# Performance work log

Measured on AMD Instinct MI355X. Metric: run time of the kernel, lower is better.

Reference implementation:

```python
import jax, jax.numpy as jnp
import numpy as np

SUB_NO = 20
T_NO = 200
T_DATA = 200000
E_NO = 400
I_NO = 100
N_BASIS = 20
COS_SHIFT = 1.0
COS_SCALE = 5.0


def make_cos_basis():
    # (N_BASIS, T_NO) raised-cosine basis in log time
    i = jnp.arange(N_BASIS, dtype=jnp.float32)[:, None]
    phi = (jnp.pi / 2.0) * i
    x = jnp.arange(T_NO, dtype=jnp.float32)[None, :]
    raw = COS_SCALE * jnp.log(x + COS_SHIFT)
    basis = 0.5 * jnp.cos(raw - phi) + 0.5
    keep = (raw >= phi - jnp.pi) & (raw <= phi + jnp.pi)
    return jnp.where(keep, basis, 0.0)


def grouped_causal_conv(syn, kern_flipped):
    # syn: (T, sub), kern_flipped: (sub, T_NO) already time-reversed -> causal filter
    x = jnp.pad(syn.T, ((0, 0), (T_NO - 1, 0)))[None]          # (1, sub, T+T_NO-1)
    out = jax.lax.conv_general_dilated(
        x, kern_flipped[:, None, :], (1,), 'VALID',
        dimension_numbers=('NCH', 'OIH', 'NCH'),
        feature_group_count=syn.shape[1])
    return out[0].T                                             # (T, sub)


def causal_conv1(z_pad, kern_flipped):
    # z_pad: (L,), kern_flipped: (T_NO,) -> valid conv, length L - T_NO + 1
    out = jax.lax.conv_general_dilated(
        z_pad[None, None, :], kern_flipped[None, None, :], (1,), 'VALID',
        dimension_numbers=('NCH', 'OIH', 'NCH'))
    return out[0, 0]


def setup_inputs() -> dict:
    key = jax.random.key(0)
    ks = jax.random.split(key, 12)
    S_e = (jax.random.uniform(ks[0], (T_DATA, E_NO)) < 0.05).astype(jnp.float32)
    S_i = (jax.random.uniform(ks[1], (T_DATA, I_NO)) < 0.05).astype(jnp.float32)
    Z = (jax.random.uniform(ks[2], (T_DATA,)) < 0.02).astype(jnp.float32)
    # binary-tree dendrite adjacency
    C_den = np.zeros((SUB_NO, SUB_NO), dtype=np.int32)
    for c in range(1, SUB_NO):
        C_den[(c - 1) // 2, c] = 1
    C_den = jnp.asarray(C_den)
    e_asn = np.asarray(jax.random.randint(ks[3], (E_NO,), 0, SUB_NO))
    i_asn = np.asarray(jax.random.randint(ks[4], (I_NO,), 0, SUB_NO))
    C_syn_e = np.zeros((SUB_NO, E_NO), dtype=np.float32); C_syn_e[e_asn, np.arange(E_NO)] = 1.0
    C_syn_i = np.zeros((SUB_NO, I_NO), dtype=np.float32); C_syn_i[i_asn, np.arange(I_NO)] = 1.0
    W_syn_ns = jax.random.uniform(ks[5], (SUB_NO, 2)) * 0.1
    W_syn_ns = W_syn_ns.at[:, 1].multiply(-1.0)
    return {
        'S_e': S_e, 'S_i': S_i, 'Z': Z,
        'C_den': C_den,
        'C_syn_e': jnp.asarray(C_syn_e), 'C_syn_i': jnp.asarray(C_syn_i),
        'W_syn_ns': W_syn_ns,
        'Tau_syn_ns': jnp.ones((SUB_NO, 2)) * 3.0,
        'Delta_syn_ns': jnp.zeros((SUB_NO, 2)),
        'W_syn_s': jax.random.normal(ks[6], (SUB_NO, N_BASIS, 2)) * 0.01,
        'W_sub_ns': jnp.ones(SUB_NO) * 0.1,
        'W_sub_s': jnp.ones(SUB_NO) * 0.1,
        'V_o': jax.random.normal(ks[7], (1,)),
        'Theta_ns': jnp.zeros(SUB_NO),
        'Theta_s': jnp.zeros(SUB_NO),
        'hist_s_weights': jax.random.normal(ks[8], (N_BASIS,)) * 0.01,
        'hist_ns_weights': jax.random.normal(ks[9], (N_BASIS,)) * 0.01,
    }


def reference(S_e, S_i, Z, C_den, C_syn_e, C_syn_i, W_syn_ns, Tau_syn_ns,
              Delta_syn_ns, W_syn_s, W_sub_ns, W_sub_s, V_o, Theta_ns,
              Theta_s, hist_s_weights, hist_ns_weights):
    cos_basis = make_cos_basis()
    # --- spike_convolve ---
    syn_e = S_e @ C_syn_e.T                                     # (T, sub)
    syn_i = S_i @ C_syn_i.T
    t = jnp.arange(T_NO, dtype=jnp.float32)[None, :]
    tau_e = Tau_syn_ns[:, 0:1] ** 2
    tau_i = Tau_syn_ns[:, 1:2] ** 2
    t_e = jnp.maximum(t - Delta_syn_ns[:, 0:1], 0.0) / tau_e
    t_i = jnp.maximum(t - Delta_syn_ns[:, 1:2], 0.0) / tau_i
    e_kern_ns = t_e * jnp.exp(-t_e) * W_syn_ns[:, 0:1] ** 2      # (sub, T_NO)
    i_kern_ns = -t_i * jnp.exp(-t_i) * W_syn_ns[:, 1:2] ** 2
    e_kern_s = (W_syn_s[:, :, 0] ** 2) @ cos_basis               # (sub, T_NO)
    i_kern_s = -(W_syn_s[:, :, 1] ** 2) @ cos_basis
    filt_e_ns = grouped_causal_conv(syn_e, jnp.flip(e_kern_ns, 1))
    filt_i_ns = grouped_causal_conv(syn_i, jnp.flip(i_kern_ns, 1))
    filt_e_s = grouped_causal_conv(syn_e, jnp.flip(e_kern_s, 1))
    filt_i_s = grouped_causal_conv(syn_i, jnp.flip(i_kern_s, 1))
    syn_ns = filt_e_ns + filt_i_ns
    syn_s = filt_e_s + filt_i_s
    # --- spike-history filtering of observed root spikes Z ---
    hist_s_kern = hist_s_weights @ cos_basis                     # (T_NO,)
    hist_ns_kern = hist_ns_weights @ cos_basis
    Z_pad = jnp.pad(Z, (T_NO, 0))                                # (T + T_NO,)
    hist_ns_filt = causal_conv1(Z_pad, jnp.flip(hist_ns_kern))[:-1]  # (T,)
    hist_s_filt = causal_conv1(Z_pad, jnp.flip(hist_s_kern))[:-1]
    # --- leaf-to-root tree recursion (unrolled over SUB_NO static nodes) ---
    C_den_f = C_den.astype(syn_s.dtype)
    w_s2 = W_sub_s ** 2
    w_ns2 = W_sub_ns ** 2
    T_data = S_e.shape[0]
    s_out = jnp.zeros((T_data, SUB_NO), dtype=syn_s.dtype)
    ns_out = jnp.zeros((T_data, SUB_NO), dtype=syn_ns.dtype)
    for idx in range(SUB_NO - 1, 0, -1):
        child_s = s_out @ (C_den_f[idx] * w_s2)                  # (T,) 0 if leaf
        child_ns = ns_out @ (C_den_f[idx] * w_ns2)
        s_out = s_out.at[:, idx].set(jnp.tanh(syn_s[:, idx] + child_s + Theta_s[idx]))
        ns_out = ns_out.at[:, idx].set(jnp.tanh(syn_ns[:, idx] + child_ns + Theta_ns[idx]))
    root_child_s = s_out @ (C_den_f[0] * w_s2)
    root_child_ns = ns_out @ (C_den_f[0] * w_ns2)
    s0 = jax.nn.sigmoid(hist_s_filt + syn_s[:, 0] + root_child_s + Theta_s[0])
    ns0 = jnp.tanh(hist_ns_filt + syn_ns[:, 0] + root_child_ns + Theta_ns[0])
    final_V = ns0 * w_ns2[0] + V_o
    final_Z = s0
    out_filters = jnp.vstack((e_kern_ns, i_kern_ns, e_kern_s, i_kern_s,
                              hist_ns_kern[None, :], hist_s_kern[None, :]))
    return final_V, final_Z, out_filters
```

## Files before the change

### kernel.cpp

```cpp
#include <hip/hip_runtime.h>

#define T_DATA 200000
#define E_NO 400
#define I_NO 100
#define SUB_NO 20
#define N_BASIS 20
#define T_NO 200

typedef unsigned short u16;
typedef unsigned int u32;
typedef unsigned long long u64;
typedef _Float16 hf;
typedef _Float16 half2_t __attribute__((ext_vector_type(2)));

#define WS_KT    0
#define WS_MASKS 33600
#define WS_SYNEI 65536
#define WS_SNS   (WS_SYNEI + 16000000)
#define WS_SS    (WS_SNS + 8000000)
#define WS_HF    (WS_SS + 8000000)

__device__ __forceinline__ u16 f2h(float f) {
    hf h = (hf)f; u16 b; __builtin_memcpy(&b, &h, 2); return b;
}
__device__ __forceinline__ float h2f(u16 b) {
    hf h; __builtin_memcpy(&h, &b, 2); return (float)h;
}
__device__ __forceinline__ float dot2(u32 a, u32 b, float c) {
    half2_t ha, hb;
    __builtin_memcpy(&ha, &a, 4);
    __builtin_memcpy(&hb, &b, 4);
    return __builtin_amdgcn_fdot2(ha, hb, c, false);
}
__device__ __forceinline__ float fast_tanh(float x) {
    x = fminf(fmaxf(x, -15.f), 15.f);
    float e = __expf(2.f * x);
    return 1.f - 2.f / (e + 1.f);
}
__device__ __forceinline__ float fast_sigmoid(float x) {
    x = fminf(fmaxf(x, -30.f), 30.f);
    return 1.f / (1.f + __expf(-x));
}

__global__ __launch_bounds__(256) void k_setup(
    const float* __restrict__ Wns, const float* __restrict__ Tau,
    const float* __restrict__ Del, const float* __restrict__ Wsyns,
    const float* __restrict__ HwS, const float* __restrict__ HwNS,
    const float* __restrict__ Cse, const float* __restrict__ Csi,
    uint2* __restrict__ ktap, u32* __restrict__ masks32,
    float* __restrict__ outF)
{
    __shared__ float cb[N_BASIS * T_NO];
    __shared__ u32 m32[480];
    const int tid = threadIdx.x;
    const int b = blockIdx.x;
    const float PI = 3.14159265358979323846f;

    if (b == 21) {
        for (int k = tid; k < 480; k += 256) m32[k] = 0;
        __syncthreads();
        for (int j = tid; j < E_NO; j += 256) {
            int a = 0;
            for (int s = 0; s < SUB_NO; ++s)
                if (Cse[s * E_NO + j] > 0.5f) a = s;
            int ch = j >> 8, r = j & 255, ln = r >> 2, cp = r & 3;
            int widx = (a * 8 + ch * 4 + cp) * 2 + (ln >> 5);
            atomicOr(&m32[widx], 1u << (ln & 31));
        }
        for (int j = tid; j < I_NO; j += 256) {
            int a = 0;
            for (int s = 0; s < SUB_NO; ++s)
                if (Csi[s * I_NO + j] > 0.5f) a = s;
            int ln = j >> 2, cp = j & 3;
            int widx = 320 + (a * 4 + cp) * 2 + (ln >> 5);
            atomicOr(&m32[widx], 1u << (ln & 31));
        }
        __syncthreads();
        for (int k = tid; k < 480; k += 256) masks32[k] = m32[k];
        return;
    }

    for (int it = tid; it < N_BASIS * T_NO; it += 256) {
        int bb = it / T_NO, j = it - bb * T_NO;
        float phi = 1.57079632679489662f * (float)bb;
        float raw = 5.0f * logf((float)j + 1.0f);
        float v = 0.f;
        if (raw >= phi - PI && raw <= phi + PI) v = 0.5f * cosf(raw - phi) + 0.5f;
        cb[it] = v;
    }
    __syncthreads();

    if (b < 20) {
        const int s = b;
        if (tid < T_NO) {
            const int j = tid;
            float tau_e = Tau[s * 2 + 0]; tau_e *= tau_e;
            float tau_i = Tau[s * 2 + 1]; tau_i *= tau_i;
            float de = Del[s * 2 + 0], di = Del[s * 2 + 1];
            float we = Wns[s * 2 + 0]; we *= we;
            float wi = Wns[s * 2 + 1]; wi *= wi;
            float te = fmaxf((float)j - de, 0.f) / tau_e;
            float ti = fmaxf((float)j - di, 0.f) / tau_i;
            float eNs = te * expf(-te) * we;
            float iNs = -ti * expf(-ti) * wi;
            float eS = 0.f, iS = 0.f;
            for (int bb = 0; bb < N_BASIS; ++bb) {
                float w0 = Wsyns[(s * N_BASIS + bb) * 2 + 0];
                float w1 = Wsyns[(s * N_BASIS + bb) * 2 + 1];
                float c = cb[bb * T_NO + j];
                eS += w0 * w0 * c;
                iS -= w1 * w1 * c;
            }
            int it = s * T_NO + j;
            outF[it]         = eNs;
            outF[4000 + it]  = iNs;
            outF[8000 + it]  = eS;
            outF[12000 + it] = iS;
            u32 pN = (u32)f2h(eNs) | ((u32)f2h(iNs) << 16);
            u32 pS = (u32)f2h(eS)  | ((u32)f2h(iS)  << 16);
            ktap[s * T_NO + (199 - j)] = make_uint2(pN, pS);
        }
    } else {
        if (tid < T_NO) {
            const int j = tid;
            float hn = 0.f, hs = 0.f;
            for (int bb = 0; bb < N_BASIS; ++bb) {
                float c = cb[bb * T_NO + j];
                hn += HwNS[bb] * c;
                hs += HwS[bb] * c;
            }
            outF[16000 + j] = hn;
            outF[16200 + j] = hs;
            ktap[20 * T_NO + (199 - j)] = make_uint2((u32)f2h(hn), (u32)f2h(hs));
        }
    }
}

__global__ __launch_bounds__(256) void k_spikes(
    const float* __restrict__ Se, const float* __restrict__ Si,
    const u64* __restrict__ masks,
    u32* __restrict__ synEI)
{
    __shared__ u16 tile[4][40 * 18];
    const int tid = threadIdx.x;
    const int wv = tid >> 6, lane = tid & 63;
    const int t0 = (blockIdx.x * 4 + wv) * 16;

    u64 me0 = 0, me1 = 0, me2 = 0, me3 = 0, me4 = 0, me5 = 0, me6 = 0, me7 = 0;
    u64 mi0 = 0, mi1 = 0, mi2 = 0, mi3 = 0;
    if (lane < 20) {
        const u64* mp = masks + lane * 8;
        me0 = mp[0]; me1 = mp[1]; me2 = mp[2]; me3 = mp[3];
        me4 = mp[4]; me5 = mp[5]; me6 = mp[6]; me7 = mp[7];
    } else if (lane < 40) {
        const u64* mp = masks + 160 + (lane - 20) * 4;
        mi0 = mp[0]; mi1 = mp[1]; mi2 = mp[2]; mi3 = mp[3];
    }
    u16* tw = tile[wv];

#pragma unroll 2
    for (int tt = 0; tt < 16; ++tt) {
        const int t = t0 + tt;
        const float4* rE = (const float4*)(Se + (size_t)t * E_NO);
        const float4* rI = (const float4*)(Si + (size_t)t * I_NO);
        float4 e0 = rE[lane];
        float4 e1 = make_float4(0.f, 0.f, 0.f, 0.f);
        if (lane < 36) e1 = rE[64 + lane];
        float4 i0 = make_float4(0.f, 0.f, 0.f, 0.f);
        if (lane < 25) i0 = rI[lane];
        u64 b0 = __ballot(e0.x != 0.f);
        u64 b1 = __ballot(e0.y != 0.f);
        u64 b2 = __ballot(e0.z != 0.f);
        u64 b3 = __ballot(e0.w != 0.f);
        u64 b4 = __ballot(e1.x != 0.f);
        u64 b5 = __ballot(e1.y != 0.f);
        u64 b6 = __ballot(e1.z != 0.f);
        u64 b7 = __ballot(e1.w != 0.f);
        u64 c0 = __ballot(i0.x != 0.f);
        u64 c1 = __ballot(i0.y != 0.f);
        u64 c2 = __ballot(i0.z != 0.f);
        u64 c3 = __ballot(i0.w != 0.f);
        if (lane < 20) {
            int c = __popcll(b0 & me0) + __popcll(b1 & me1)
                  + __popcll(b2 & me2) + __popcll(b3 & me3)
                  + __popcll(b4 & me4) + __popcll(b5 & me5)
                  + __popcll(b6 & me6) + __popcll(b7 & me7);
            tw[lane * 18 + tt] = (u16)c;
        } else if (lane < 40) {
            int c = __popcll(c0 & mi0) + __popcll(c1 & mi1)
                  + __popcll(c2 & mi2) + __popcll(c3 & mi3);
            tw[lane * 18 + tt] = (u16)c;
        }
    }
    asm volatile("s_waitcnt lgkmcnt(0)" ::: "memory");

    if (lane < 16) {
#pragma unroll
        for (int s = 0; s < 20; ++s) {
            float fe = (float)tw[s * 18 + lane];
            float fi = (float)tw[(20 + s) * 18 + lane];
            u32 v = (u32)f2h(fe) | ((u32)f2h(fi) << 16);
            synEI[(size_t)s * T_DATA + t0 + lane] = v;
        }
    }
}

#define TT 512
#define WROW 712
__global__ __launch_bounds__(256) void k_conv(
    const u32* __restrict__ synEI, const float* __restrict__ Z,
    const uint2* __restrict__ ktap,
    u16* __restrict__ synNSb, u16* __restrict__ synSb,
    float2* __restrict__ hfilt)
{
    __shared__ __align__(16) u32 wEI[4 * WROW];
    const int tid = threadIdx.x;
    const int t0 = blockIdx.x * TT;
    const int g  = blockIdx.y;
    const int W0 = t0 - 200;

    if (g < 5) {
        for (int q = tid; q < 4 * 178; q += 256) {
            int row = q / 178, c = q - row * 178;
            int s = g * 4 + row;
            const u32* src = synEI + (size_t)s * T_DATA;
            u32* dst = wEI + row * WROW + c * 4;
            int gg = W0 + c * 4;
            if (gg >= 0 && gg + 4 <= T_DATA) {
                *(uint4*)dst = *(const uint4*)(src + gg);
            } else {
#pragma unroll
                for (int e = 0; e < 4; ++e) {
                    int t = gg + e;
                    dst[e] = (t >= 0 && t < T_DATA) ? src[t] : 0u;
                }
            }
        }
    } else {
        for (int q = tid; q < 3 * 178; q += 256)
            ((uint4*)(wEI + WROW))[q] = make_uint4(0, 0, 0, 0);
        for (int c = tid; c < 178; c += 256) {
            int gg = W0 + c * 4;
            u32 o[4];
#pragma unroll
            for (int e = 0; e < 4; ++e) {
                int t = gg + e;
                float z = (t >= 0 && t < T_DATA) ? Z[t] : 0.f;
                o[e] = (u32)f2h(z);
            }
            *(uint4*)(wEI + c * 4) = make_uint4(o[0], o[1], o[2], o[3]);
        }
    }
    __syncthreads();

    const int wv = tid >> 6;
    const int slot = tid & 63;
    const int bT = slot * 8;
    const u32* row = wEI + wv * WROW;
    const int su = (g < 5) ? (g * 4 + wv) : 20;
    const uint2* kt = ktap + (size_t)__builtin_amdgcn_readfirstlane(su) * T_NO;

    float aN[8], aS[8];
#pragma unroll
    for (int m = 0; m < 8; ++m) { aN[m] = 0.f; aS[m] = 0.f; }

    u32 x[16];
    {
        uint4 wA = *(const uint4*)(row + bT);
        uint4 wB = *(const uint4*)(row + bT + 4);
        uint4 wC = *(const uint4*)(row + bT + 8);
        uint4 wD = *(const uint4*)(row + bT + 12);
        x[0]=wA.x; x[1]=wA.y; x[2]=wA.z; x[3]=wA.w;
        x[4]=wB.x; x[5]=wB.y; x[6]=wB.z; x[7]=wB.w;
        x[8]=wC.x; x[9]=wC.y; x[10]=wC.z; x[11]=wC.w;
        x[12]=wD.x; x[13]=wD.y; x[14]=wD.z; x[15]=wD.w;
    }

#pragma unroll 1
    for (int jj = 0; jj <= 192; jj += 8) {
        uint2 kp[8];
#pragma unroll
        for (int k = 0; k < 8; ++k) kp[k] = kt[jj + k];
#pragma unroll
        for (int k = 0; k < 8; ++k) {
#pragma unroll
            for (int m = 0; m < 8; ++m) {
                aN[m] = dot2(x[m + 1 + k], kp[k].x, aN[m]);
                aS[m] = dot2(x[m + 1 + k], kp[k].y, aS[m]);
            }
        }
        if (jj < 192) {
#pragma unroll
            for (int i = 0; i < 8; ++i) x[i] = x[i + 8];
            uint4 nA = *(const uint4*)(row + bT + jj + 16);
            uint4 nB = *(const uint4*)(row + bT + jj + 20);
            x[8]=nA.x; x[9]=nA.y; x[10]=nA.z; x[11]=nA.w;
            x[12]=nB.x; x[13]=nB.y; x[14]=nB.z; x[15]=nB.w;
        }
    }

    if (g < 5) {
        const int s = g * 4 + wv;
        const int t = t0 + bT;
        u32 w0 = (u32)f2h(aN[0]) | ((u32)f2h(aN[1]) << 16);
        u32 w1 = (u32)f2h(aN[2]) | ((u32)f2h(aN[3]) << 16);
        u32 w2 = (u32)f2h(aN[4]) | ((u32)f2h(aN[5]) << 16);
        u32 w3 = (u32)f2h(aN[6]) | ((u32)f2h(aN[7]) << 16);
        u32 v0 = (u32)f2h(aS[0]) | ((u32)f2h(aS[1]) << 16);
        u32 v1 = (u32)f2h(aS[2]) | ((u32)f2h(aS[3]) << 16);
        u32 v2 = (u32)f2h(aS[4]) | ((u32)f2h(aS[5]) << 16);
        u32 v3 = (u32)f2h(aS[6]) | ((u32)f2h(aS[7]) << 16);
        if (t + 8 <= T_DATA) {
            *(uint4*)(synNSb + (size_t)s * T_DATA + t) = make_uint4(w0, w1, w2, w3);
            *(uint4*)(synSb  + (size_t)s * T_DATA + t) = make_uint4(v0, v1, v2, v3);
        } else if (t < T_DATA) {
            for (int m = 0; m < 8 && t + m < T_DATA; ++m) {
                synNSb[(size_t)s * T_DATA + t + m] = f2h(aN[m]);
                synSb[(size_t)s * T_DATA + t + m] = f2h(aS[m]);
            }
        }
    } else if (wv == 0) {
#pragma unroll
        for (int m = 0; m < 8; ++m) {
            int tt = t0 + bT + m + 1;
            if (tt < T_DATA) hfilt[tt] = make_float2(aN[m], aS[m]);
        }
        if (blockIdx.x == 0 && tid == 0) hfilt[0] = make_float2(0.f, 0.f);
    }
}

#define CT 256
__global__ __launch_bounds__(256) void k_tree(
    const u16* __restrict__ synNSb, const u16* __restrict__ synSb,
    const float2* __restrict__ hfilt,
    const int* __restrict__ Cden,
    const float* __restrict__ WsubNS, const float* __restrict__ WsubS,
    const float* __restrict__ Vo, const float* __restrict__ ThNS,
    const float* __restrict__ ThS,
    float* __restrict__ outV, float* __restrict__ outZ)
{
    __shared__ __align__(16) u16 lNS[SUB_NO * CT];
    __shared__ __align__(16) u16 lS[SUB_NO * CT];
    __shared__ float AS[SUB_NO][SUB_NO], AN[SUB_NO][SUB_NO];
    __shared__ float ths[SUB_NO], thn[SUB_NO];
    __shared__ float wn20s, vos;
    const int tid = threadIdx.x;
    const int t0 = blockIdx.x * CT;

    for (int q = tid; q < 1280; q += 256) {
        int arr = (q >= 640) ? 1 : 0;
        int qq = q - arr * 640;
        int row = qq >> 5, c = qq & 31;
        const u16* src = (arr ? synSb : synNSb) + (size_t)row * T_DATA;
        u16* dst = (arr ? lS : lNS) + row * CT + c * 8;
        int gg = t0 + c * 8;
        if (gg + 8 <= T_DATA) {
            *(uint4*)dst = *(const uint4*)(src + gg);
        } else {
            for (int e = 0; e < 8; ++e) {
                int t = gg + e;
                dst[e] = (t < T_DATA) ? src[t] : (u16)0;
            }
        }
    }
    for (int k = tid; k < SUB_NO * SUB_NO; k += 256) {
        int idx = k / SUB_NO, c = k - idx * SUB_NO;
        float m = (float)Cden[k];
        float wsv = WsubS[c];
        float wnv = WsubNS[c];
        AS[idx][c] = m * wsv * wsv;
        AN[idx][c] = m * wnv * wnv;
    }
    if (tid < SUB_NO) { ths[tid] = ThS[tid]; thn[tid] = ThNS[tid]; }
    if (tid == 0) {
        float w = WsubNS[0];
        wn20s = w * w;
        vos = Vo[0];
    }
    __syncthreads();

    const int t = t0 + tid;
    float2 hf = make_float2(0.f, 0.f);
    if (t < T_DATA) hf = hfilt[t];

    float vs[SUB_NO], vn[SUB_NO];
#pragma unroll
    for (int c = 0; c < SUB_NO; ++c) { vs[c] = 0.f; vn[c] = 0.f; }
#pragma unroll
    for (int idx = SUB_NO - 1; idx >= 1; --idx) {
        float cs = 0.f, cn = 0.f;
#pragma unroll
        for (int c = 0; c < SUB_NO; ++c) {
            cs = fmaf(AS[idx][c], vs[c], cs);
            cn = fmaf(AN[idx][c], vn[c], cn);
        }
        float synS_v = h2f(lS[idx * CT + tid]);
        float synN_v = h2f(lNS[idx * CT + tid]);
        vs[idx] = fast_tanh(synS_v + cs + ths[idx]);
        vn[idx] = fast_tanh(synN_v + cn + thn[idx]);
    }
    float cs0 = 0.f, cn0 = 0.f;
#pragma unroll
    for (int c = 0; c < SUB_NO; ++c) {
        cs0 = fmaf(AS[0][c], vs[c], cs0);
        cn0 = fmaf(AN[0][c], vn[c], cn0);
    }
    float s0  = fast_sigmoid(hf.y + h2f(lS[tid]) + cs0 + ths[0]);
    float ns0 = fast_tanh(hf.x + h2f(lNS[tid]) + cn0 + thn[0]);

    if (t < T_DATA) {
        outV[t] = ns0 * wn20s + vos;
        outZ[t] = s0;
    }
}

extern "C" void kernel_launch(void* const* d_in, const int* in_sizes, int n_in,
                              void* d_out, int out_size, void* d_ws, size_t ws_size,
                              hipStream_t stream)
{
    const float* Se    = (const float*)d_in[0];
    const float* Si    = (const float*)d_in[1];
    const float* Z     = (const float*)d_in[2];
    const int*   Cden  = (const int*)d_in[3];
    const float* Cse   = (const float*)d_in[4];
    const float* Csi   = (const float*)d_in[5];
    const float* Wns   = (const float*)d_in[6];
    const float* Tau   = (const float*)d_in[7];
    const float* Del   = (const float*)d_in[8];
    const float* Wsyns = (const float*)d_in[9];
    const float* WsubNS= (const float*)d_in[10];
    const float* WsubS = (const float*)d_in[11];
    const float* Vo    = (const float*)d_in[12];
    const float* ThNS  = (const float*)d_in[13];
    const float* ThS   = (const float*)d_in[14];
    const float* HwS   = (const float*)d_in[15];
    const float* HwNS  = (const float*)d_in[16];

    char* ws = (char*)d_ws;
    uint2*  ktap  = (uint2*)(ws + WS_KT);
    u64*    masks = (u64*)(ws + WS_MASKS);
    u32*    synEI = (u32*)(ws + WS_SYNEI);
    u16*    synNSb= (u16*)(ws + WS_SNS);
    u16*    synSb = (u16*)(ws + WS_SS);
    float2* hfilt = (float2*)(ws + WS_HF);

    float* outV = (float*)d_out;
    float* outZ = outV + T_DATA;
    float* outF = outV + 2 * T_DATA;

    k_setup<<<22, 256, 0, stream>>>(Wns, Tau, Del, Wsyns, HwS, HwNS, Cse, Csi,
                                    ktap, (u32*)masks, outF);
    k_spikes<<<3125, 256, 0, stream>>>(Se, Si, masks, synEI);
    dim3 gc((T_DATA + TT - 1) / TT, 6);
    k_conv<<<gc, 256, 0, stream>>>(synEI, Z, ktap, synNSb, synSb, hfilt);
    k_tree<<<(T_DATA + CT - 1) / CT, 256, 0, stream>>>(
        synNSb, synSb, hfilt, Cden, WsubNS, WsubS, Vo, ThNS, ThS,
        outV, outZ);
}
```

Measured before the change: 606.1 us.

## Fuse causal convolution and dendritic tree into one kernel via shared memory

Merges the convolution kernel and the tree-recursion kernel into a single kernel. Each block handles 256 timesteps, loops over subunit groups, and keeps the packed half-precision conv results in LDS instead of writing and re-reading intermediate arrays in global memory. This removes a launch and global traffic for the synNS, synS and history-filter arrays. In exchange, each block re-reads a 200-sample halo per 256 outputs, so there is more redundant halo loading. Each thread now computes 4 outputs instead of 8, and the history filter is stored in fp16 rather than fp32.

```diff
diff --git a/kernel.cpp b/kernel.cpp
--- a/kernel.cpp
+++ b/kernel.cpp
@@ -16,9 +16,6 @@
 #define WS_KT    0
 #define WS_MASKS 33600
 #define WS_SYNEI 65536
-#define WS_SNS   (WS_SYNEI + 16000000)
-#define WS_SS    (WS_SNS + 8000000)
-#define WS_HF    (WS_SS + 8000000)
 
 __device__ __forceinline__ u16 f2h(float f) {
     hf h = (hf)f; u16 b; __builtin_memcpy(&b, &h, 2); return b;
@@ -205,164 +202,27 @@
     }
 }
 
-#define TT 512
-#define WROW 712
-__global__ __launch_bounds__(256) void k_conv(
+#define FT 256
+#define FW 456
+__global__ __launch_bounds__(256) void k_fused(
     const u32* __restrict__ synEI, const float* __restrict__ Z,
     const uint2* __restrict__ ktap,
-    u16* __restrict__ synNSb, u16* __restrict__ synSb,
-    float2* __restrict__ hfilt)
-{
-    __shared__ __align__(16) u32 wEI[4 * WROW];
-    const int tid = threadIdx.x;
-    const int t0 = blockIdx.x * TT;
-    const int g  = blockIdx.y;
-    const int W0 = t0 - 200;
-
-    if (g < 5) {
-        for (int q = tid; q < 4 * 178; q += 256) {
-            int row = q / 178, c = q - row * 178;
-            int s = g * 4 + row;
-            const u32* src = synEI + (size_t)s * T_DATA;
-            u32* dst = wEI + row * WROW + c * 4;
-            int gg = W0 + c * 4;
-            if (gg >= 0 && gg + 4 <= T_DATA) {
-                *(uint4*)dst = *(const uint4*)(src + gg);
-            } else {
-#pragma unroll
-                for (int e = 0; e < 4; ++e) {
-                    int t = gg + e;
-                    dst[e] = (t >= 0 && t < T_DATA) ? src[t] : 0u;
-                }
-            }
-        }
-    } else {
-        for (int q = tid; q < 3 * 178; q += 256)
-            ((uint4*)(wEI + WROW))[q] = make_uint4(0, 0, 0, 0);
-        for (int c = tid; c < 178; c += 256) {
-            int gg = W0 + c * 4;
-            u32 o[4];
-#pragma unroll
-            for (int e = 0; e < 4; ++e) {
-                int t = gg + e;
-                float z = (t >= 0 && t < T_DATA) ? Z[t] : 0.f;
-                o[e] = (u32)f2h(z);
-            }
-            *(uint4*)(wEI + c * 4) = make_uint4(o[0], o[1], o[2], o[3]);
-        }
-    }
-    __syncthreads();
-
-    const int wv = tid >> 6;
-    const int slot = tid & 63;
-    const int bT = slot * 8;
-    const u32* row = wEI + wv * WROW;
-    const int su = (g < 5) ? (g * 4 + wv) : 20;
-    const uint2* kt = ktap + (size_t)__builtin_amdgcn_readfirstlane(su) * T_NO;
-
-    float aN[8], aS[8];
-#pragma unroll
-    for (int m = 0; m < 8; ++m) { aN[m] = 0.f; aS[m] = 0.f; }
-
-    u32 x[16];
-    {
-        uint4 wA = *(const uint4*)(row + bT);
-        uint4 wB = *(const uint4*)(row + bT + 4);
-        uint4 wC = *(const uint4*)(row + bT + 8);
-        uint4 wD = *(const uint4*)(row + bT + 12);
-        x[0]=wA.x; x[1]=wA.y; x[2]=wA.z; x[3]=wA.w;
-        x[4]=wB.x; x[5]=wB.y; x[6]=wB.z; x[7]=wB.w;
-        x[8]=wC.x; x[9]=wC.y; x[10]=wC.z; x[11]=wC.w;
-        x[12]=wD.x; x[13]=wD.y; x[14]=wD.z; x[15]=wD.w;
-    }
-
-#pragma unroll 1
-    for (int jj = 0; jj <= 192; jj += 8) {
-        uint2 kp[8];
-#pragma unroll
-        for (int k = 0; k < 8; ++k) kp[k] = kt[jj + k];
-#pragma unroll
-        for (int k = 0; k < 8; ++k) {
-#pragma unroll
-            for (int m = 0; m < 8; ++m) {
-                aN[m] = dot2(x[m + 1 + k], kp[k].x, aN[m]);
-                aS[m] = dot2(x[m + 1 + k], kp[k].y, aS[m]);
-            }
-        }
-        if (jj < 192) {
-#pragma unroll
-            for (int i = 0; i < 8; ++i) x[i] = x[i + 8];
-            uint4 nA = *(const uint4*)(row + bT + jj + 16);
-            uint4 nB = *(const uint4*)(row + bT + jj + 20);
-            x[8]=nA.x; x[9]=nA.y; x[10]=nA.z; x[11]=nA.w;
-            x[12]=nB.x; x[13]=nB.y; x[14]=nB.z; x[15]=nB.w;
-        }
-    }
-
-    if (g < 5) {
-        const int s = g * 4 + wv;
-        const int t = t0 + bT;
-        u32 w0 = (u32)f2h(aN[0]) | ((u32)f2h(aN[1]) << 16);
-        u32 w1 = (u32)f2h(aN[2]) | ((u32)f2h(aN[3]) << 16);
-        u32 w2 = (u32)f2h(aN[4]) | ((u32)f2h(aN[5]) << 16);
-        u32 w3 = (u32)f2h(aN[6]) | ((u32)f2h(aN[7]) << 16);
-        u32 v0 = (u32)f2h(aS[0]) | ((u32)f2h(aS[1]) << 16);
-        u32 v1 = (u32)f2h(aS[2]) | ((u32)f2h(aS[3]) << 16);
-        u32 v2 = (u32)f2h(aS[4]) | ((u32)f2h(aS[5]) << 16);
-        u32 v3 = (u32)f2h(aS[6]) | ((u32)f2h(aS[7]) << 16);
-        if (t + 8 <= T_DATA) {
-            *(uint4*)(synNSb + (size_t)s * T_DATA + t) = make_uint4(w0, w1, w2, w3);
-            *(uint4*)(synSb  + (size_t)s * T_DATA + t) = make_uint4(v0, v1, v2, v3);
-        } else if (t < T_DATA) {
-            for (int m = 0; m < 8 && t + m < T_DATA; ++m) {
-                synNSb[(size_t)s * T_DATA + t + m] = f2h(aN[m]);
-                synSb[(size_t)s * T_DATA + t + m] = f2h(aS[m]);
-            }
-        }
-    } else if (wv == 0) {
-#pragma unroll
-        for (int m = 0; m < 8; ++m) {
-            int tt = t0 + bT + m + 1;
-            if (tt < T_DATA) hfilt[tt] = make_float2(aN[m], aS[m]);
-        }
-        if (blockIdx.x == 0 && tid == 0) hfilt[0] = make_float2(0.f, 0.f);
-    }
-}
-
-#define CT 256
-__global__ __launch_bounds__(256) void k_tree(
-    const u16* __restrict__ synNSb, const u16* __restrict__ synSb,
-    const float2* __restrict__ hfilt,
     const int* __restrict__ Cden,
     const float* __restrict__ WsubNS, const float* __restrict__ WsubS,
     const float* __restrict__ Vo, const float* __restrict__ ThNS,
     const float* __restrict__ ThS,
     float* __restrict__ outV, float* __restrict__ outZ)
 {
-    __shared__ __align__(16) u16 lNS[SUB_NO * CT];
-    __shared__ __align__(16) u16 lS[SUB_NO * CT];
+    __shared__ __align__(16) u32 wEI[4 * FW];
+    __shared__ __align__(16) u32 res[21 * FT];
     __shared__ float AS[SUB_NO][SUB_NO], AN[SUB_NO][SUB_NO];
     __shared__ float ths[SUB_NO], thn[SUB_NO];
     __shared__ float wn20s, vos;
     const int tid = threadIdx.x;
-    const int t0 = blockIdx.x * CT;
-
-    for (int q = tid; q < 1280; q += 256) {
-        int arr = (q >= 640) ? 1 : 0;
-        int qq = q - arr * 640;
-        int row = qq >> 5, c = qq & 31;
-        const u16* src = (arr ? synSb : synNSb) + (size_t)row * T_DATA;
-        u16* dst = (arr ? lS : lNS) + row * CT + c * 8;
-        int gg = t0 + c * 8;
-        if (gg + 8 <= T_DATA) {
-            *(uint4*)dst = *(const uint4*)(src + gg);
-        } else {
-            for (int e = 0; e < 8; ++e) {
-                int t = gg + e;
-                dst[e] = (t < T_DATA) ? src[t] : (u16)0;
-            }
-        }
-    }
+    const int wv = tid >> 6, lane = tid & 63;
+    const int t0 = blockIdx.x * FT;
+    const int W0 = t0 - 200;
+
     for (int k = tid; k < SUB_NO * SUB_NO; k += 256) {
         int idx = k / SUB_NO, c = k - idx * SUB_NO;
         float m = (float)Cden[k];
@@ -377,11 +237,92 @@
         wn20s = w * w;
         vos = Vo[0];
     }
+
+#pragma unroll 1
+    for (int p = 0; p < 6; ++p) {
+        __syncthreads();
+        if (p < 5) {
+            for (int q = tid; q < 4 * 114; q += 256) {
+                int row = q / 114, c = q - row * 114;
+                int s = p * 4 + row;
+                const u32* src = synEI + (size_t)s * T_DATA;
+                u32* dst = wEI + row * FW + c * 4;
+                int gg = W0 + c * 4;
+                if (gg >= 0 && gg + 4 <= T_DATA) {
+                    *(uint4*)dst = *(const uint4*)(src + gg);
+                } else {
+#pragma unroll
+                    for (int e = 0; e < 4; ++e) {
+                        int t = gg + e;
+                        dst[e] = (t >= 0 && t < T_DATA) ? src[t] : 0u;
+                    }
+                }
+            }
+        } else {
+            for (int c = tid; c < FW; c += 256) {
+                int t = W0 + c - 1;
+                float z = (t >= 0 && t < T_DATA) ? Z[t] : 0.f;
+                wEI[c] = (u32)f2h(z);
+            }
+        }
+        __syncthreads();
+
+        const int su = p * 4 + wv;
+        if (p < 5 || wv == 0) {
+            const uint2* kt = ktap +
+                (size_t)__builtin_amdgcn_readfirstlane(su) * T_NO;
+            const u32* row = wEI + ((p < 5) ? wv * FW : 0);
+            const int bT = lane * 4;
+
+            float aN[4], aS[4];
+#pragma unroll
+            for (int m = 0; m < 4; ++m) { aN[m] = 0.f; aS[m] = 0.f; }
+
+            u32 x[12];
+            {
+                uint4 wA = *(const uint4*)(row + bT);
+                uint4 wB = *(const uint4*)(row + bT + 4);
+                uint4 wC = *(const uint4*)(row + bT + 8);
+                x[0]=wA.x; x[1]=wA.y; x[2]=wA.z; x[3]=wA.w;
+                x[4]=wB.x; x[5]=wB.y; x[6]=wB.z; x[7]=wB.w;
+                x[8]=wC.x; x[9]=wC.y; x[10]=wC.z; x[11]=wC.w;
+            }
+
+#pragma unroll 1
+            for (int jj = 0; jj <= 192; jj += 8) {
+                uint2 kp[8];
+#pragma unroll
+                for (int k = 0; k < 8; ++k) kp[k] = kt[jj + k];
+#pragma unroll
+                for (int k = 0; k < 8; ++k) {
+#pragma unroll
+                    for (int m = 0; m < 4; ++m) {
+                        aN[m] = dot2(x[m + 1 + k], kp[k].x, aN[m]);
+                        aS[m] = dot2(x[m + 1 + k], kp[k].y, aS[m]);
+                    }
+                }
+                if (jj < 192) {
+#pragma unroll
+                    for (int i = 0; i < 4; ++i) x[i] = x[i + 8];
+                    uint4 nA = *(const uint4*)(row + bT + jj + 12);
+                    uint4 nB = *(const uint4*)(row + bT + jj + 16);
+                    x[4]=nA.x; x[5]=nA.y; x[6]=nA.z; x[7]=nA.w;
+                    x[8]=nB.x; x[9]=nB.y; x[10]=nB.z; x[11]=nB.w;
+                }
+            }
+            u32 o0 = (u32)f2h(aN[0]) | ((u32)f2h(aS[0]) << 16);
+            u32 o1 = (u32)f2h(aN[1]) | ((u32)f2h(aS[1]) << 16);
+            u32 o2 = (u32)f2h(aN[2]) | ((u32)f2h(aS[2]) << 16);
+            u32 o3 = (u32)f2h(aN[3]) | ((u32)f2h(aS[3]) << 16);
+            *(uint4*)&res[su * FT + bT] = make_uint4(o0, o1, o2, o3);
+        }
+    }
     __syncthreads();
 
     const int t = t0 + tid;
-    float2 hf = make_float2(0.f, 0.f);
-    if (t < T_DATA) hf = hfilt[t];
+    u32 hh = res[20 * FT + tid];
+    float hn = h2f((u16)(hh & 0xffffu));
+    float hs = h2f((u16)(hh >> 16));
 
     float vs[SUB_NO], vn[SUB_NO];
 #pragma unroll
@@ -394,8 +335,9 @@
             cs = fmaf(AS[idx][c], vs[c], cs);
             cn = fmaf(AN[idx][c], vn[c], cn);
         }
-        float synS_v = h2f(lS[idx * CT + tid]);
-        float synN_v = h2f(lNS[idx * CT + tid]);
+        u32 r = res[idx * FT + tid];
+        float synN_v = h2f((u16)(r & 0xffffu));
+        float synS_v = h2f((u16)(r >> 16));
         vs[idx] = fast_tanh(synS_v + cs + ths[idx]);
         vn[idx] = fast_tanh(synN_v + cn + thn[idx]);
     }
@@ -405,8 +347,9 @@
         cs0 = fmaf(AS[0][c], vs[c], cs0);
         cn0 = fmaf(AN[0][c], vn[c], cn0);
     }
-    float s0  = fast_sigmoid(hf.y + h2f(lS[tid]) + cs0 + ths[0]);
-    float ns0 = fast_tanh(hf.x + h2f(lNS[tid]) + cn0 + thn[0]);
+    u32 r0 = res[tid];
+    float s0  = fast_sigmoid(hs + h2f((u16)(r0 >> 16)) + cs0 + ths[0]);
+    float ns0 = fast_tanh(hn + h2f((u16)(r0 & 0xffffu)) + cn0 + thn[0]);
 
     if (t < T_DATA) {
         outV[t] = ns0 * wn20s + vos;
@@ -440,9 +383,6 @@
     uint2*  ktap  = (uint2*)(ws + WS_KT);
     u64*    masks = (u64*)(ws + WS_MASKS);
     u32*    synEI = (u32*)(ws + WS_SYNEI);
-    u16*    synNSb= (u16*)(ws + WS_SNS);
-    u16*    synSb = (u16*)(ws + WS_SS);
-    float2* hfilt = (float2*)(ws + WS_HF);
 
     float* outV = (float*)d_out;
     float* outZ = outV + T_DATA;
@@ -451,9 +391,6 @@
     k_setup<<<22, 256, 0, stream>>>(Wns, Tau, Del, Wsyns, HwS, HwNS, Cse, Csi,
                                     ktap, (u32*)masks, outF);
     k_spikes<<<3125, 256, 0, stream>>>(Se, Si, masks, synEI);
-    dim3 gc((T_DATA + TT - 1) / TT, 6);
-    k_conv<<<gc, 256, 0, stream>>>(synEI, Z, ktap, synNSb, synSb, hfilt);
-    k_tree<<<(T_DATA + CT - 1) / CT, 256, 0, stream>>>(
-        synNSb, synSb, hfilt, Cden, WsubNS, WsubS, Vo, ThNS, ThS,
-        outV, outZ);
-}
+    k_fused<<<(T_DATA + FT - 1) / FT, 256, 0, stream>>>(
+        synEI, Z, ktap, Cden, WsubNS, WsubS, Vo, ThNS, ThS, outV, outZ);
+}
```

New measurement: 625.5 us. 3.2% more time.
